# Performance work log

Measured on AMD Instinct MI355X. Metric: run time of the kernel, lower is better.

## Reference

```python
import jax, jax.numpy as jnp
import numpy as np

# Static architecture sizes (see shape_source)
B, H, W, NCH = 64, 64, 64, 3
K = 2                     # kernel at every stage
D = 20                    # bond_dim == virtual_dim
OUT = 10                  # output_dim
P1 = (H // K) * (W // K)          # 1024 patches, stage 1
P2 = P1 // (K * K)                # 256 patches, stage 2
P3 = P2 // (K * K)                # 64 patches, stage 3
FP = 2 * K * K                    # feature_dim per stage = 2*ker^2 = 8
FF = 2 * D                        # feature_dim of final MPS = 2*virtual_dim


def _unfold(x, k):
    # torch: x.unfold(2,k,k).unfold(3,k,k).reshape(b, k*k, -1, C)
    b, C, Hh, Ww = x.shape
    v = x.reshape(b, C, Hh // k, k, Ww // k, k).transpose(0, 1, 2, 4, 3, 5)
    return v.reshape(b, k * k, -1, C)   # [b, k^2, P, C] (raw reshape, faithful)


def _batchnorm(y, g, bb, eps=1e-5):
    # BatchNorm1d(C) on [b, C, L], training mode (batch stats), affine
    mu = jnp.mean(y, axis=(0, 2), keepdims=True)
    var = jnp.var(y, axis=(0, 2), keepdims=True)
    return g[None, :, None] * (y - mu) * jax.lax.rsqrt(var + eps) + bb[None, :, None]


def _mps(x, cores, label, alpha, omega):
    # Batched tensor-train contraction over independent per-patch MPS modules.
    # x:     [b, Fraw, P, S]  (S sites per MPS, P independent MPS modules)
    # cores: [P, S, 2*Fraw, D, D], label: [O, D, D], alpha/omega: [D]
    phi = jnp.concatenate([x, 1.0 - x], axis=1)              # [b, F, P, S]
    M = jnp.einsum('bfps,psfij->spbij', phi, cores)          # per-site transfer mats
    def step(c, m):
        return jnp.einsum('pbij,pbjk->pbik', c, m), None
    eye = jnp.broadcast_to(jnp.eye(cores.shape[-1], dtype=x.dtype), M.shape[1:])
    tot, _ = jax.lax.scan(step, eye, M)                      # [P, b, D, D]
    return jnp.einsum('i,pbij,ojk,k->bpo', alpha, tot, label, omega)  # [b, P, O]


def _cores(key, P, S, F):
    # near-identity init; sum_f phi_f = Fraw = F/2, so scale eye by 2/F
    return (jnp.eye(D, dtype=jnp.float32) * (2.0 / F)
            + 0.01 * jax.random.normal(key, (P, S, F, D, D), jnp.float32))


def setup_inputs() -> dict:
    ks = jax.random.split(jax.random.key(0), 12)
    one, zero = jnp.ones((D,), jnp.float32), jnp.zeros
    return {
        'x': jax.random.normal(ks[0], (B, NCH, H, W), jnp.float32),
        'cores1': _cores(ks[1], P1, NCH, FP),
        'label1': 0.1 * jax.random.normal(ks[2], (D, D, D), jnp.float32),
        'alpha1': one, 'omega1': one,
        'g1': jnp.ones((P1,), jnp.float32), 'b1': zero((P1,), jnp.float32),
        'cores2': _cores(ks[3], P2, D, FP),
        'label2': 0.1 * jax.random.normal(ks[4], (D, D, D), jnp.float32),
        'alpha2': one, 'omega2': one,
        'g2': jnp.ones((P2,), jnp.float32), 'b2': zero((P2,), jnp.float32),
        'cores3': _cores(ks[5], P3, D, FP),
        'label3': 0.1 * jax.random.normal(ks[6], (D, D, D), jnp.float32),
        'alpha3': one, 'omega3': one,
        'g3': jnp.ones((P3,), jnp.float32), 'b3': zero((P3,), jnp.float32),
        'coresF': _cores(ks[7], 1, P3, FF),
        'labelF': 0.1 * jax.random.normal(ks[8], (OUT, D, D), jnp.float32),
        'alphaF': one, 'omegaF': one,
    }


def reference(x, cores1, label1, alpha1, omega1, g1, b1,
              cores2, label2, alpha2, omega2, g2, b2,
              cores3, label3, alpha3, omega3, g3, b3,
              coresF, labelF, alphaF, omegaF):
    b = x.shape[0]
    u = _unfold(x, K)                              # [b, 4, P1, 3]
    y = _mps(u, cores1, label1, alpha1, omega1)    # [b, P1, D]
    y = _batchnorm(y, g1, b1).reshape(b, D, H // K, W // K)   # raw view, faithful
    u = _unfold(y, K)                              # [b, 4, P2, D]
    y = _mps(u, cores2, label2, alpha2, omega2)    # [b, P2, D]
    y = _batchnorm(y, g2, b2).reshape(b, D, H // (K * K), W // (K * K))
    u = _unfold(y, K)                              # [b, 4, P3, D]
    y = _mps(u, cores3, label3, alpha3, omega3)    # [b, P3, D]
    y = _batchnorm(y, g3, b3)
    y = jnp.transpose(y, (0, 2, 1))                # [b, D, P3]
    out = _mps(y[:, :, None, :], coresF, labelF, alphaF, omegaF)[:, 0, :]
    return out                                     # [b, OUT]
```

## Files before the change

### kernel.cpp

```cpp
#include <hip/hip_runtime.h>
#include <hip/hip_bf16.h>

typedef __attribute__((ext_vector_type(4))) float f32x4;
typedef __attribute__((ext_vector_type(8))) short s16x8;

static __device__ __forceinline__ short f2bf(float x) {
  __hip_bfloat16 h = __float2bfloat16(x);
  return *reinterpret_cast<short*>(&h);
}

__global__ void k_setup(const float* __restrict__ l1, const float* __restrict__ o1,
                        const float* __restrict__ l2, const float* __restrict__ o2,
                        const float* __restrict__ l3, const float* __restrict__ o3,
                        const float* __restrict__ lF, const float* __restrict__ oF,
                        float* __restrict__ ws) {
  int e = blockIdx.x * blockDim.x + threadIdx.x;
  if (e >= 1400) return;
  const float* lab; const float* om; float* dst; int idx;
  if (e < 400)       { lab = l1; om = o1; dst = ws;        idx = e; }
  else if (e < 800)  { lab = l2; om = o2; dst = ws + 400;  idx = e - 400; }
  else if (e < 1200) { lab = l3; om = o3; dst = ws + 800;  idx = e - 800; }
  else               { lab = lF; om = oF; dst = ws + 1200; idx = e - 1200; }
  int o = idx / 20, j = idx % 20;
  float a = 0.f;
  for (int k = 0; k < 20; ++k) a += lab[o*400 + j*20 + k] * om[k];
  dst[idx] = a;
}

template<int STAGE>
__global__ __launch_bounds__(256)
void k_mps(const float* __restrict__ xsrc, const float* __restrict__ ysrc,
           const float* __restrict__ cores, const float* __restrict__ alpha,
           const float* __restrict__ Lw, const float* __restrict__ gam,
           const float* __restrict__ bet, float* __restrict__ yout) {
  constexpr int S = (STAGE == 1) ? 3 : 20;
  __shared__ float u4[S][64][4];
  __shared__ __align__(16) short Cl[2][32][168];
  __shared__ __align__(16) float vls[64][36];
  __shared__ float redA[4], redB[4], stats[2];

  const int p = blockIdx.x, t = threadIdx.x;
  const int b = t & 63, q = t >> 6;
  const int m = b & 15, quad = b >> 4;
  const int bl = q * 16 + m;

  float rA[8], rB[8];
  const bool two = (t < 144);
  {
    const float* cs = cores + (size_t)p * S * 3200;
#pragma unroll
    for (int g = 0; g < 8; ++g) rA[g] = cs[g * 400 + t];
    if (two) {
#pragma unroll
      for (int g = 0; g < 8; ++g) rB[g] = cs[g * 400 + 256 + t];
    }
  }

  {
    int* cz = (int*)&Cl[0][0][0];
    for (int i = t; i < 5376; i += 256) cz[i] = 0;
    for (int i = t; i < 64 * 36; i += 256) {
      int col = i % 36;
      vls[i / 36][col] = (col < 20) ? alpha[col] : 0.f;
    }
  }

  for (int k = 0; k < S; ++k) {
    float val;
    if (STAGE == 1) {
      int L = q * 3072 + p * 3 + k;
      int c = L >> 12, r = L & 4095;
      int hh = 2 * (r >> 7) + ((r >> 1) & 1);
      int ww = 2 * ((r >> 2) & 31) + (r & 1);
      val = xsrc[(b * 3 + c) * 4096 + hh * 64 + ww];
    } else if (STAGE == 2) {
      int L = q * 5120 + p * 20 + k;
      int c = L >> 10, r = L & 1023;
      int f = c * 1024 + (2 * (r >> 6) + ((r >> 1) & 1)) * 32
                        + (2 * ((r >> 2) & 15) + (r & 1));
      val = ysrc[f * 64 + b];
    } else {
      int L = q * 1280 + p * 20 + k;
      int c = L >> 8, r = L & 255;
      int f = c * 256 + (2 * (r >> 5) + ((r >> 1) & 1)) * 16
                       + (2 * ((r >> 2) & 7) + (r & 1));
      val = ysrc[f * 64 + b];
    }
    u4[k][b][q] = val;
  }
  __syncthreads();

  auto writeC = [&](int buf, int e, const float* r) {
    int i = e / 20, j = e % 20;
    Cl[buf][j][      i] = f2bf(r[0] - r[4]);
    Cl[buf][j][ 32 + i] = f2bf(r[1] - r[5]);
    Cl[buf][j][ 64 + i] = f2bf(r[2] - r[6]);
    Cl[buf][j][ 96 + i] = f2bf(r[3] - r[7]);
    float cs = r[4] + r[5] + r[6] + r[7];
    if (i == j) cs -= 1.f;
    Cl[buf][j][128 + i] = f2bf(cs);
  };

  writeC(0, t, rA);
  if (two) writeC(0, t + 256, rB);
  if (S > 1) {
    const float* cs = cores + ((size_t)p * S + 1) * 3200;
#pragma unroll
    for (int g = 0; g < 8; ++g) rA[g] = cs[g * 400 + t];
    if (two) {
#pragma unroll
      for (int g = 0; g < 8; ++g) rB[g] = cs[g * 400 + 256 + t];
    }
  }
  __syncthreads();

  for (int s = 0; s < S; ++s) {
    const int cur = s & 1;
    const float4 uu = *(const float4*)&u4[s][bl][0];
    const float4 va = *(const float4*)&vls[bl][quad * 8];
    const float4 vb = *(const float4*)&vls[bl][quad * 8 + 4];
    const float vv[8] = {va.x, va.y, va.z, va.w, vb.x, vb.y, vb.z, vb.w};
    const float um[5] = {uu.x, uu.y, uu.z, uu.w, 1.f};

    f32x4 acc0 = {0.f, 0.f, 0.f, 0.f};
    f32x4 acc1 = {0.f, 0.f, 0.f, 0.f};
#pragma unroll
    for (int kt = 0; kt < 5; ++kt) {
      s16x8 aF;
#pragma unroll
      for (int j2 = 0; j2 < 8; ++j2) aF[j2] = f2bf(vv[j2] * um[kt]);
      const s16x8 bF0 = *(const s16x8*)&Cl[cur][m][kt * 32 + quad * 8];
      const s16x8 bF1 = *(const s16x8*)&Cl[cur][m + 16][kt * 32 + quad * 8];
      acc0 = __builtin_amdgcn_mfma_f32_16x16x32_bf16(aF, bF0, acc0, 0, 0, 0);
      acc1 = __builtin_amdgcn_mfma_f32_16x16x32_bf16(aF, bF1, acc1, 0, 0, 0);
    }

    if (s + 1 < S) {
      writeC(cur ^ 1, t, rA);
      if (two) writeC(cur ^ 1, t + 256, rB);
      if (s + 2 < S) {
        const float* cs = cores + ((size_t)p * S + s + 2) * 3200;
#pragma unroll
        for (int g = 0; g < 8; ++g) rA[g] = cs[g * 400 + t];
        if (two) {
#pragma unroll
          for (int g = 0; g < 8; ++g) rB[g] = cs[g * 400 + 256 + t];
        }
      }
    }
    __syncthreads();

#pragma unroll
    for (int r = 0; r < 4; ++r) {
      const int bb = q * 16 + quad * 4 + r;
      vls[bb][m] += acc0[r];
    }
    if (m < 4) {
#pragma unroll
      for (int r = 0; r < 4; ++r) {
        const int bb = q * 16 + quad * 4 + r;
        vls[bb][m + 16] += acc1[r];
      }
    }
    __syncthreads();
  }

  float vf[20];
  {
    const float4 v0 = *(const float4*)&vls[b][0];
    const float4 v1 = *(const float4*)&vls[b][4];
    const float4 v2 = *(const float4*)&vls[b][8];
    const float4 v3 = *(const float4*)&vls[b][12];
    const float4 v4 = *(const float4*)&vls[b][16];
    vf[0]=v0.x; vf[1]=v0.y; vf[2]=v0.z; vf[3]=v0.w;
    vf[4]=v1.x; vf[5]=v1.y; vf[6]=v1.z; vf[7]=v1.w;
    vf[8]=v2.x; vf[9]=v2.y; vf[10]=v2.z; vf[11]=v2.w;
    vf[12]=v3.x; vf[13]=v3.y; vf[14]=v3.z; vf[15]=v3.w;
    vf[16]=v4.x; vf[17]=v4.y; vf[18]=v4.z; vf[19]=v4.w;
  }
  float yo[5];
  float s1 = 0.f, s2 = 0.f;
#pragma unroll
  for (int jj = 0; jj < 5; ++jj) {
    int o = q * 5 + jj;
    float a = 0.f;
#pragma unroll
    for (int j = 0; j < 20; ++j) a = fmaf(vf[j], Lw[o * 20 + j], a);
    yo[jj] = a; s1 += a; s2 += a * a;
  }
#pragma unroll
  for (int off = 32; off > 0; off >>= 1) {
    s1 += __shfl_down(s1, off); s2 += __shfl_down(s2, off);
  }
  if (b == 0) { redA[q] = s1; redB[q] = s2; }
  __syncthreads();
  if (t == 0) {
    float S1 = redA[0] + redA[1] + redA[2] + redA[3];
    float S2 = redB[0] + redB[1] + redB[2] + redB[3];
    float mu = S1 * (1.f / 1280.f);
    float var = S2 * (1.f / 1280.f) - mu * mu;
    if (var < 0.f) var = 0.f;
    stats[0] = mu; stats[1] = var;
  }
  __syncthreads();
  float mu = stats[0], var = stats[1];
  float scale = gam[p] / sqrtf(var + 1e-5f);
  float shift = bet[p] - mu * scale;
#pragma unroll
  for (int jj = 0; jj < 5; ++jj) {
    int o = q * 5 + jj;
    yout[(p * 20 + o) * 64 + b] = fmaf(yo[jj], scale, shift);
  }
}

__global__ __launch_bounds__(256)
void k_f1(const float* __restrict__ y3n, const float* __restrict__ coresF,
          float* __restrict__ PP) {
  const int bid = blockIdx.x;
  const int b = bid >> 3, c = bid & 7;
  const int t = threadIdx.x;
  __shared__ float ybuf[8][20];
  __shared__ float M[400];
  __shared__ float Pb[2][400];
  if (t < 160) ybuf[t / 20][t % 20] = y3n[(c * 160 + t) * 64 + b];
  __syncthreads();
  int cur = 0;
  for (int s = 0; s < 8; ++s) {
    const float* cf = coresF + (size_t)(c * 8 + s) * 16000;
    for (int e = t; e < 400; e += 256) {
      float m = 0.f;
#pragma unroll
      for (int g = 0; g < 20; ++g) {
        float lo = cf[g * 400 + e];
        float hi = cf[(g + 20) * 400 + e];
        m += fmaf(ybuf[s][g], lo - hi, hi);
      }
      M[e] = m;
    }
    __syncthreads();
    if (s == 0) {
      for (int e = t; e < 400; e += 256) Pb[0][e] = M[e];
    } else {
      for (int e = t; e < 400; e += 256) {
        int i = e / 20, j = e % 20;
        float a = 0.f;
#pragma unroll
        for (int k = 0; k < 20; ++k)
          a = fmaf(Pb[cur][i * 20 + k], M[k * 20 + j], a);
        Pb[cur ^ 1][e] = a;
      }
      cur ^= 1;
    }
    __syncthreads();
  }
  for (int e = t; e < 400; e += 256) PP[(size_t)bid * 400 + e] = Pb[cur][e];
}

__global__ __launch_bounds__(256)
void k_f2(const float* __restrict__ PP, const float* __restrict__ alphaF,
          const float* __restrict__ LwF, float* __restrict__ out) {
  const int b = blockIdx.x, t = threadIdx.x;
  __shared__ float Pb[2][400];
  __shared__ float M[400];
  __shared__ float va[20];
  for (int e = t; e < 400; e += 256) Pb[0][e] = PP[(size_t)b * 3200 + e];
  int cur = 0;
  for (int c = 1; c < 8; ++c) {
    for (int e = t; e < 400; e += 256) M[e] = PP[(size_t)b * 3200 + c * 400 + e];
    __syncthreads();
    for (int e = t; e < 400; e += 256) {
      int i = e / 20, j = e % 20;
      float a = 0.f;
#pragma unroll
      for (int k = 0; k < 20; ++k) a = fmaf(Pb[cur][i * 20 + k], M[k * 20 + j], a);
      Pb[cur ^ 1][e] = a;
    }
    cur ^= 1;
    __syncthreads();
  }
  if (t < 20) {
    float a = 0.f;
#pragma unroll
    for (int i = 0; i < 20; ++i) a = fmaf(alphaF[i], Pb[cur][i * 20 + t], a);
    va[t] = a;
  }
  __syncthreads();
  if (t < 10) {
    float a = 0.f;
#pragma unroll
    for (int j = 0; j < 20; ++j) a = fmaf(va[j], LwF[t * 20 + j], a);
    out[b * 10 + t] = a;
  }
}

extern "C" void kernel_launch(void* const* d_in, const int* in_sizes, int n_in,
                              void* d_out, int out_size, void* d_ws, size_t ws_size,
                              hipStream_t stream) {
  const float* x      = (const float*)d_in[0];
  const float* cores1 = (const float*)d_in[1];
  const float* label1 = (const float*)d_in[2];
  const float* alpha1 = (const float*)d_in[3];
  const float* omega1 = (const float*)d_in[4];
  const float* g1     = (const float*)d_in[5];
  const float* b1     = (const float*)d_in[6];
  const float* cores2 = (const float*)d_in[7];
  const float* label2 = (const float*)d_in[8];
  const float* alpha2 = (const float*)d_in[9];
  const float* omega2 = (const float*)d_in[10];
  const float* g2     = (const float*)d_in[11];
  const float* b2     = (const float*)d_in[12];
  const float* cores3 = (const float*)d_in[13];
  const float* label3 = (const float*)d_in[14];
  const float* alpha3 = (const float*)d_in[15];
  const float* omega3 = (const float*)d_in[16];
  const float* g3     = (const float*)d_in[17];
  const float* b3     = (const float*)d_in[18];
  const float* coresF = (const float*)d_in[19];
  const float* labelF = (const float*)d_in[20];
  const float* alphaF = (const float*)d_in[21];
  const float* omegaF = (const float*)d_in[22];

  float* ws  = (float*)d_ws;
  float* Lw1 = ws;
  float* Lw2 = ws + 400;
  float* Lw3 = ws + 800;
  float* LwF = ws + 1200;
  float* yn1 = ws + 1400;
  float* yn2 = yn1 + 1310720;
  float* yn3 = yn2 + 327680;
  float* PP  = yn3 + 81920;
  float* out = (float*)d_out;

  k_setup<<<6, 256, 0, stream>>>(label1, omega1, label2, omega2,
                                 label3, omega3, labelF, omegaF, ws);
  k_mps<1><<<1024, 256, 0, stream>>>(x, nullptr, cores1, alpha1, Lw1, g1, b1, yn1);
  k_mps<2><<<256, 256, 0, stream>>>(nullptr, yn1, cores2, alpha2, Lw2, g2, b2, yn2);
  k_mps<3><<<64, 256, 0, stream>>>(nullptr, yn2, cores3, alpha3, Lw3, g3, b3, yn3);
  k_f1<<<512, 256, 0, stream>>>(yn3, coresF, PP);
  k_f2<<<64, 256, 0, stream>>>(PP, alphaF, LwF, out);
}
```

Measured before the change: 256.4 us.

## Fold label·omega setup into MPS kernels and deepen core prefetch, merge syncs

Removes the separate k_setup launch; each MPS block and k_f2 now computes its own label·omega vector into shared memory. The core-prefetch pipeline deepens from one to two sites ahead using two register sets, with the loop unrolled by two so buffer parity is static. Per site the two __syncthreads shrink to one, and one barrier before the loop is dropped. This trades a kernel launch and barriers for redundant label compute per block and higher register pressure, and the single barrier may leave a race on vls/Cl between sites.

```diff
diff --git a/kernel.cpp b/kernel.cpp
--- a/kernel.cpp
+++ b/kernel.cpp
@@ -7,36 +7,20 @@
 static __device__ __forceinline__ short f2bf(float x) {
   __hip_bfloat16 h = __float2bfloat16(x);
   return *reinterpret_cast<short*>(&h);
-}
-
-__global__ void k_setup(const float* __restrict__ l1, const float* __restrict__ o1,
-                        const float* __restrict__ l2, const float* __restrict__ o2,
-                        const float* __restrict__ l3, const float* __restrict__ o3,
-                        const float* __restrict__ lF, const float* __restrict__ oF,
-                        float* __restrict__ ws) {
-  int e = blockIdx.x * blockDim.x + threadIdx.x;
-  if (e >= 1400) return;
-  const float* lab; const float* om; float* dst; int idx;
-  if (e < 400)       { lab = l1; om = o1; dst = ws;        idx = e; }
-  else if (e < 800)  { lab = l2; om = o2; dst = ws + 400;  idx = e - 400; }
-  else if (e < 1200) { lab = l3; om = o3; dst = ws + 800;  idx = e - 800; }
-  else               { lab = lF; om = oF; dst = ws + 1200; idx = e - 1200; }
-  int o = idx / 20, j = idx % 20;
-  float a = 0.f;
-  for (int k = 0; k < 20; ++k) a += lab[o*400 + j*20 + k] * om[k];
-  dst[idx] = a;
 }
 
 template<int STAGE>
 __global__ __launch_bounds__(256)
 void k_mps(const float* __restrict__ xsrc, const float* __restrict__ ysrc,
            const float* __restrict__ cores, const float* __restrict__ alpha,
-           const float* __restrict__ Lw, const float* __restrict__ gam,
-           const float* __restrict__ bet, float* __restrict__ yout) {
+           const float* __restrict__ label, const float* __restrict__ omega,
+           const float* __restrict__ gam, const float* __restrict__ bet,
+           float* __restrict__ yout) {
   constexpr int S = (STAGE == 1) ? 3 : 20;
-  __shared__ float u4[S][64][4];
+  __shared__ __align__(16) float u4[S][64][4];
   __shared__ __align__(16) short Cl[2][32][168];
   __shared__ __align__(16) float vls[64][36];
+  __shared__ float Lw_l[400];
   __shared__ float redA[4], redB[4], stats[2];
 
   const int p = blockIdx.x, t = threadIdx.x;
@@ -44,16 +28,23 @@
   const int m = b & 15, quad = b >> 4;
   const int bl = q * 16 + m;
 
-  float rA[8], rB[8];
   const bool two = (t < 144);
-  {
-    const float* cs = cores + (size_t)p * S * 3200;
-#pragma unroll
-    for (int g = 0; g < 8; ++g) rA[g] = cs[g * 400 + t];
-    if (two) {
-#pragma unroll
-      for (int g = 0; g < 8; ++g) rB[g] = cs[g * 400 + 256 + t];
-    }
+  const float* cbase = cores + (size_t)p * S * 3200;
+
+  float p0A[8], p0B[8], p1A[8], p1B[8];
+#pragma unroll
+  for (int g = 0; g < 8; ++g) p0A[g] = cbase[g * 400 + t];
+  if (two) {
+#pragma unroll
+    for (int g = 0; g < 8; ++g) p0B[g] = cbase[g * 400 + 256 + t];
+  }
+
+  for (int e = t; e < 400; e += 256) {
+    int o = e / 20, j = e % 20;
+    float a = 0.f;
+#pragma unroll
+    for (int k = 0; k < 20; ++k) a = fmaf(label[o * 400 + j * 20 + k], omega[k], a);
+    Lw_l[e] = a;
   }
 
   {
@@ -88,7 +79,6 @@
     }
     u4[k][b][q] = val;
   }
-  __syncthreads();
 
   auto writeC = [&](int buf, int e, const float* r) {
     int i = e / 20, j = e % 20;
@@ -100,22 +90,23 @@
     if (i == j) cs -= 1.f;
     Cl[buf][j][128 + i] = f2bf(cs);
   };
-
-  writeC(0, t, rA);
-  if (two) writeC(0, t + 256, rB);
-  if (S > 1) {
-    const float* cs = cores + ((size_t)p * S + 1) * 3200;
+  auto loadSite = [&](int s, float (&rA)[8], float (&rB)[8]) {
+    const float* cs = cbase + (size_t)s * 3200;
 #pragma unroll
     for (int g = 0; g < 8; ++g) rA[g] = cs[g * 400 + t];
     if (two) {
 #pragma unroll
       for (int g = 0; g < 8; ++g) rB[g] = cs[g * 400 + 256 + t];
     }
-  }
-  __syncthreads();
-
-  for (int s = 0; s < S; ++s) {
-    const int cur = s & 1;
+  };
+
+  writeC(0, t, p0A);
+  if (two) writeC(0, t + 256, p0B);
+  if (S > 1) loadSite(1, p0A, p0B);
+  if (S > 2) loadSite(2, p1A, p1B);
+  __syncthreads();
+
+  auto site_step = [&](int s, int cur, float (&rA)[8], float (&rB)[8]) {
     const float4 uu = *(const float4*)&u4[s][bl][0];
     const float4 va = *(const float4*)&vls[bl][quad * 8];
     const float4 vb = *(const float4*)&vls[bl][quad * 8 + 4];
@@ -138,31 +129,21 @@
     if (s + 1 < S) {
       writeC(cur ^ 1, t, rA);
       if (two) writeC(cur ^ 1, t + 256, rB);
-      if (s + 2 < S) {
-        const float* cs = cores + ((size_t)p * S + s + 2) * 3200;
-#pragma unroll
-        for (int g = 0; g < 8; ++g) rA[g] = cs[g * 400 + t];
-        if (two) {
-#pragma unroll
-          for (int g = 0; g < 8; ++g) rB[g] = cs[g * 400 + 256 + t];
-        }
-      }
-    }
-    __syncthreads();
-
-#pragma unroll
-    for (int r = 0; r < 4; ++r) {
-      const int bb = q * 16 + quad * 4 + r;
-      vls[bb][m] += acc0[r];
-    }
+      if (s + 3 < S) loadSite(s + 3, rA, rB);
+    }
+
+#pragma unroll
+    for (int r = 0; r < 4; ++r) vls[q * 16 + quad * 4 + r][m] += acc0[r];
     if (m < 4) {
 #pragma unroll
-      for (int r = 0; r < 4; ++r) {
-        const int bb = q * 16 + quad * 4 + r;
-        vls[bb][m + 16] += acc1[r];
-      }
-    }
-    __syncthreads();
+      for (int r = 0; r < 4; ++r) vls[q * 16 + quad * 4 + r][m + 16] += acc1[r];
+    }
+    __syncthreads();
+  };
+
+  for (int s = 0; s < S; s += 2) {
+    site_step(s, 0, p0A, p0B);
+    if (s + 1 < S) site_step(s + 1, 1, p1A, p1B);
   }
 
   float vf[20];
@@ -185,7 +166,7 @@
     int o = q * 5 + jj;
     float a = 0.f;
 #pragma unroll
-    for (int j = 0; j < 20; ++j) a = fmaf(vf[j], Lw[o * 20 + j], a);
+    for (int j = 0; j < 20; ++j) a = fmaf(vf[j], Lw_l[o * 20 + j], a);
     yo[jj] = a; s1 += a; s2 += a * a;
   }
 #pragma unroll
@@ -258,11 +239,20 @@
 
 __global__ __launch_bounds__(256)
 void k_f2(const float* __restrict__ PP, const float* __restrict__ alphaF,
-          const float* __restrict__ LwF, float* __restrict__ out) {
+          const float* __restrict__ labelF, const float* __restrict__ omegaF,
+          float* __restrict__ out) {
   const int b = blockIdx.x, t = threadIdx.x;
   __shared__ float Pb[2][400];
   __shared__ float M[400];
   __shared__ float va[20];
+  __shared__ float LwF_l[200];
+  if (t < 200) {
+    int o = t / 20, j = t % 20;
+    float a = 0.f;
+#pragma unroll
+    for (int k = 0; k < 20; ++k) a = fmaf(labelF[o * 400 + j * 20 + k], omegaF[k], a);
+    LwF_l[t] = a;
+  }
   for (int e = t; e < 400; e += 256) Pb[0][e] = PP[(size_t)b * 3200 + e];
   int cur = 0;
   for (int c = 1; c < 8; ++c) {
@@ -288,7 +278,7 @@
   if (t < 10) {
     float a = 0.f;
 #pragma unroll
-    for (int j = 0; j < 20; ++j) a = fmaf(va[j], LwF[t * 20 + j], a);
+    for (int j = 0; j < 20; ++j) a = fmaf(va[j], LwF_l[t * 20 + j], a);
     out[b * 10 + t] = a;
   }
 }
@@ -321,21 +311,15 @@
   const float* omegaF = (const float*)d_in[22];
 
   float* ws  = (float*)d_ws;
-  float* Lw1 = ws;
-  float* Lw2 = ws + 400;
-  float* Lw3 = ws + 800;
-  float* LwF = ws + 1200;
-  float* yn1 = ws + 1400;
+  float* yn1 = ws;
   float* yn2 = yn1 + 1310720;
   float* yn3 = yn2 + 327680;
   float* PP  = yn3 + 81920;
   float* out = (float*)d_out;
 
-  k_setup<<<6, 256, 0, stream>>>(label1, omega1, label2, omega2,
-                                 label3, omega3, labelF, omegaF, ws);
-  k_mps<1><<<1024, 256, 0, stream>>>(x, nullptr, cores1, alpha1, Lw1, g1, b1, yn1);
-  k_mps<2><<<256, 256, 0, stream>>>(nullptr, yn1, cores2, alpha2, Lw2, g2, b2, yn2);
-  k_mps<3><<<64, 256, 0, stream>>>(nullptr, yn2, cores3, alpha3, Lw3, g3, b3, yn3);
+  k_mps<1><<<1024, 256, 0, stream>>>(x, nullptr, cores1, alpha1, label1, omega1, g1, b1, yn1);
+  k_mps<2><<<256, 256, 0, stream>>>(nullptr, yn1, cores2, alpha2, label2, omega2, g2, b2, yn2);
+  k_mps<3><<<64, 256, 0, stream>>>(nullptr, yn2, cores3, alpha3, label3, omega3, g3, b3, yn3);
   k_f1<<<512, 256, 0, stream>>>(yn3, coresF, PP);
-  k_f2<<<64, 256, 0, stream>>>(PP, alphaF, LwF, out);
-}
+  k_f2<<<64, 256, 0, stream>>>(PP, alphaF, labelF, omegaF, out);
+}
```

Measured after the change: 255.7 us. No clear change (-0.3%).
